# Kernel tuning notes

Hardware: AMD Instinct MI355X
Metric: run time of the kernel (lower is better)

Reference implementation:

```python
import jax, jax.numpy as jnp
import numpy as np

B, S, D, H = 4, 2048, 1024, 16
DEPTH = D // H
NEG = -1000000000.0


def setup_inputs() -> dict:
    key = jax.random.key(0)
    ks = jax.random.split(key, 11)
    scale = 1.0 / np.sqrt(D)
    return {
        "q": jax.random.normal(ks[0], (B, S, D), jnp.float32),
        "k": jax.random.normal(ks[1], (B, S, D), jnp.float32),
        "v": jax.random.normal(ks[2], (B, S, D), jnp.float32),
        "wq_w": jax.random.normal(ks[3], (D, D), jnp.float32) * scale,
        "wq_b": jax.random.normal(ks[4], (D,), jnp.float32) * 0.01,
        "wk_w": jax.random.normal(ks[5], (D, D), jnp.float32) * scale,
        "wk_b": jax.random.normal(ks[6], (D,), jnp.float32) * 0.01,
        "wv_w": jax.random.normal(ks[7], (D, D), jnp.float32) * scale,
        "wv_b": jax.random.normal(ks[8], (D,), jnp.float32) * 0.01,
        "dense_w": jax.random.normal(ks[9], (D, D), jnp.float32) * scale,
        "dense_b": jax.random.normal(ks[10], (D,), jnp.float32) * 0.01,
    }


def _split_heads(x):
    # (B, S, D) -> (B, H, S, depth)
    b, s, _ = x.shape
    return x.reshape(b, s, H, DEPTH).transpose(0, 2, 1, 3)


def reference(q, k, v, wq_w, wq_b, wk_w, wk_b, wv_w, wv_b, dense_w, dense_b):
    b, s, _ = q.shape
    qh = _split_heads(q @ wq_w.T + wq_b)
    kh = _split_heads(k @ wk_w.T + wk_b)
    vh = _split_heads(v @ wv_w.T + wv_b)
    logits = jnp.einsum('bhqd,bhkd->bhqk', qh, kh) / np.sqrt(DEPTH).astype(np.float32)
    # additive causal mask (strict upper triangle = -1e9)
    mask = jnp.where(jnp.triu(jnp.ones((s, s), jnp.float32), k=1) == 1.0, NEG, 0.0)
    logits = logits + mask
    attn = jax.nn.softmax(logits, axis=-1)
    out = jnp.einsum('bhqk,bhkd->bhqd', attn, vh)
    out = out.transpose(0, 2, 1, 3).reshape(b, s, D)
    return out @ dense_w.T + dense_b
```

## Files before the change

### kernel.cpp

```cpp
#include <hip/hip_runtime.h>
#include <hip/hip_bf16.h>


typedef __attribute__((ext_vector_type(8))) short bf16x8;
typedef __attribute__((ext_vector_type(4))) float f32x4;
typedef __attribute__((ext_vector_type(8))) unsigned short u16x8;

#define MFMA16(a, b, c) __builtin_amdgcn_mfma_f32_16x16x32_bf16(a, b, c, 0, 0, 0)

#define GLOAD_LDS16(gp, lp)                                                    \
  __builtin_amdgcn_global_load_lds(                                            \
      (const __attribute__((address_space(1))) void*)(gp),                     \
      (__attribute__((address_space(3))) void*)(lp), 16, 0, 0)

__device__ __forceinline__ unsigned short f2bf(float f) {
  union { float f; unsigned u; } x; x.f = f;
  unsigned u = x.u;
  return (unsigned short)((u + 0x7fffu + ((u >> 16) & 1u)) >> 16);
}

__device__ __forceinline__ unsigned pk2(float a, float b) {
  union { __hip_bfloat162 h; unsigned u; } cv;
  cv.h = __float22bfloat162_rn(float2{a, b});
  return cv.u;
}

__global__ __launch_bounds__(256) void convert_kernel(
    const float* __restrict__ q, const float* __restrict__ k,
    const float* __restrict__ v, const float* __restrict__ wq,
    const float* __restrict__ wk, const float* __restrict__ wv,
    const float* __restrict__ wd, const float* __restrict__ bq,
    const float* __restrict__ bk, const float* __restrict__ bv,
    unsigned short* __restrict__ dst, float* __restrict__ bias_pack) {
  const size_t tid0 = (size_t)blockIdx.x * blockDim.x + threadIdx.x;
  const size_t nthreads = (size_t)gridDim.x * blockDim.x;
  if (tid0 < 3072) {
    bias_pack[tid0] = tid0 < 1024 ? bq[tid0]
                     : (tid0 < 2048 ? bk[tid0 - 1024] : bv[tid0 - 2048]);
  }
  const size_t NQ = 8192ull * 1024;
  const size_t NW = 1024ull * 1024;
  const size_t total_chunks = (3 * NQ + 4 * NW) / 8;
  for (size_t c = tid0; c < total_chunks; c += nthreads) {
    const size_t e = c * 8;
    const float* src;
    if (e < NQ) src = q + e;
    else if (e < 2 * NQ) src = k + (e - NQ);
    else if (e < 3 * NQ) src = v + (e - 2 * NQ);
    else {
      const size_t we = e - 3 * NQ;
      if (we < NW) src = wq + we;
      else if (we < 2 * NW) src = wk + (we - NW);
      else if (we < 3 * NW) src = wv + (we - 2 * NW);
      else src = wd + (we - 3 * NW);
    }
    f32x4 a = *(const f32x4*)(src);
    f32x4 b = *(const f32x4*)(src + 4);
    u16x8 o;
    o[0] = f2bf(a[0]); o[1] = f2bf(a[1]); o[2] = f2bf(a[2]); o[3] = f2bf(a[3]);
    o[4] = f2bf(b[0]); o[5] = f2bf(b[1]); o[6] = f2bf(b[2]); o[7] = f2bf(b[3]);
    *(u16x8*)(dst + e) = o;
  }
}

template <int MODE>
__global__ __launch_bounds__(256) void gemm_kernel(
    const unsigned short* __restrict__ Abase,
    const unsigned short* __restrict__ Wbase,
    const float* __restrict__ biasbase, unsigned short* __restrict__ dstb,
    float* __restrict__ dstf) {
  __shared__ __attribute__((aligned(16))) unsigned short Ablk[128 * 32];
  __shared__ __attribute__((aligned(16))) unsigned short Bblk[128 * 32];
  const int z = blockIdx.z;
  const unsigned short* A = Abase + (size_t)z * (8192ull * 1024);
  const unsigned short* W = Wbase + (size_t)z * (1024ull * 1024);
  const float* bias = biasbase + (size_t)z * 1024;
  const int m0 = blockIdx.y * 128, n0 = blockIdx.x * 128;
  const int tid = threadIdx.x, lane = tid & 63, w = tid >> 6;
  const int wr = (w >> 1) * 64, wc = (w & 1) * 64;
  const int llo = lane & 15, lhi = lane >> 4;
  f32x4 acc[4][4] = {};
  const unsigned short* ag = A + (size_t)(m0 + (tid >> 2)) * 1024 + (tid & 3) * 8;
  const unsigned short* wg = W + (size_t)(n0 + (tid >> 2)) * 1024 + (tid & 3) * 8;
  unsigned short* lA = &Ablk[tid * 8];
  unsigned short* lA2 = &Ablk[2048 + tid * 8];
  unsigned short* lB = &Bblk[tid * 8];
  unsigned short* lB2 = &Bblk[2048 + tid * 8];
  for (int kt = 0; kt < 32; ++kt) {
    const int ko = kt * 32;
    if (kt) __syncthreads();
    GLOAD_LDS16(ag + ko, lA);
    GLOAD_LDS16(ag + ko + 64 * 1024, lA2);
    GLOAD_LDS16(wg + ko, lB);
    GLOAD_LDS16(wg + ko + 64 * 1024, lB2);
    __syncthreads();
    bf16x8 af[4], bfr[4];
#pragma unroll
    for (int i = 0; i < 4; ++i)
      af[i] = *(const bf16x8*)&Ablk[(wr + i * 16 + llo) * 32 + lhi * 8];
#pragma unroll
    for (int i = 0; i < 4; ++i)
      bfr[i] = *(const bf16x8*)&Bblk[(wc + i * 16 + llo) * 32 + lhi * 8];
#pragma unroll
    for (int mi = 0; mi < 4; ++mi)
#pragma unroll
      for (int ni = 0; ni < 4; ++ni)
        acc[mi][ni] = MFMA16(af[mi], bfr[ni], acc[mi][ni]);
  }
  const float osc = (MODE == 0 && z == 0) ? 0.1803368801f : 1.0f;
#pragma unroll
  for (int mi = 0; mi < 4; ++mi) {
#pragma unroll
    for (int ni = 0; ni < 4; ++ni) {
      const int n = n0 + wc + ni * 16 + llo;
      const float bv = (MODE == 2) ? 0.f : bias[n];
#pragma unroll
      for (int r = 0; r < 4; ++r) {
        const int m = m0 + wr + mi * 16 + lhi * 4 + r;
        float val = acc[mi][ni][r] + bv;
        if (MODE == 0) {
          val *= osc;
          const int b = m >> 11, s = m & 2047, h = n >> 6, d = n & 63;
          dstb[(size_t)z * (8192ull * 1024) +
               (((size_t)(b * 16 + h) * 2048 + s) * 64 + d)] = f2bf(val);
        } else if (MODE == 1) {
          dstf[(size_t)m * 1024 + n] = val;
        } else {
          val = acc[mi][ni][r] + bias[m];
          const int h = m >> 6, d = m & 63, b = n >> 11, sidx = n & 2047;
          const int t = sidx & 63;
          const int ps = (sidx & ~63) | ((t & 15) << 2) | (t >> 4);
          dstb[(((size_t)(b * 16 + h) * 64 + d) * 2048 + ps)] = f2bf(val);
        }
      }
    }
  }
}

__global__ __launch_bounds__(256, 4) void attn_kernel(
    const unsigned short* __restrict__ Qp, const unsigned short* __restrict__ Kp,
    const unsigned short* __restrict__ Vtp, unsigned short* __restrict__ attn_out) {
  __shared__ __attribute__((aligned(16))) unsigned short Klds[64 * 64];
  __shared__ __attribute__((aligned(16))) unsigned short Vt[80 * 64];
  __shared__ __attribute__((aligned(16))) unsigned short Plds[4 * 32 * 72];
  const int bh = blockIdx.x;
  const int qt = 15 - blockIdx.y;
  const int tid = threadIdx.x, lane = tid & 63, w = tid >> 6;
  const int llo = lane & 15, lhi = lane >> 4;
  const int q0 = qt * 128;
  const int qbase = q0 + w * 32;

  {
    const unsigned v16 = (tid < 16) ? 0x3F80u : 0u;
    const unsigned vv = v16 | (v16 << 16);
    *(uint2*)&Vt[64 * 64 + tid * 4] = make_uint2(vv, vv);
  }

  bf16x8 qf[2][2];
#pragma unroll
  for (int mi = 0; mi < 2; ++mi) {
    const unsigned short* qptr =
        Qp + ((size_t)bh * 2048 + qbase + mi * 16 + llo) * 64 + lhi * 8;
    qf[mi][0] = *(const bf16x8*)qptr;
    qf[mi][1] = *(const bf16x8*)(qptr + 32);
  }

  f32x4 o[2][5] = {};

  const size_t kbase = (size_t)bh * (64 * 2048);
  const int r0 = tid >> 3, r1 = r0 + 32;
  const int scb = (tid & 7) * 16;
  const int kcol0 = (scb ^ ((r0 & 7) << 4)) >> 1;
  const int kcol1 = (scb ^ ((r1 & 7) << 4)) >> 1;
  const int koff0 = r0 * 64 + kcol0, koff1 = r1 * 64 + kcol1;
  const int voff0 = r0 * 2048 + kcol0, voff1 = r1 * 2048 + kcol1;
  unsigned short* pw = &Plds[w * (32 * 72)];

  const int nkt = 2 * (qt + 1);
  for (int kt = 0; kt < nkt; ++kt) {
    const int kv0 = kt * 64;
    if (kt) __syncthreads();
    GLOAD_LDS16(Kp + kbase + (size_t)kv0 * 64 + koff0, &Klds[tid * 8]);
    GLOAD_LDS16(Kp + kbase + (size_t)kv0 * 64 + koff1, &Klds[2048 + tid * 8]);
    GLOAD_LDS16(Vtp + kbase + kv0 + voff0, &Vt[tid * 8]);
    GLOAD_LDS16(Vtp + kbase + kv0 + voff1, &Vt[2048 + tid * 8]);
    __syncthreads();
    if (kv0 > qbase + 31) continue;

    f32x4 s[2][4] = {};
#pragma unroll
    for (int b4 = 0; b4 < 4; ++b4) {
      const int row = b4 * 16 + llo;
      const int sw = (row & 7) << 3;
      const bf16x8 k0 = *(const bf16x8*)&Klds[row * 64 + ((lhi * 8) ^ sw)];
      const bf16x8 k1 = *(const bf16x8*)&Klds[row * 64 + ((32 + lhi * 8) ^ sw)];
      s[0][b4] = MFMA16(qf[0][0], k0, s[0][b4]);
      s[0][b4] = MFMA16(qf[0][1], k1, s[0][b4]);
      s[1][b4] = MFMA16(qf[1][0], k0, s[1][b4]);
      s[1][b4] = MFMA16(qf[1][1], k1, s[1][b4]);
    }

    const bool needm = (kv0 + 63 > qbase);
#pragma unroll
    for (int mi = 0; mi < 2; ++mi) {
#pragma unroll
      for (int r = 0; r < 4; ++r) {
        float sv0 = s[mi][0][r], sv1 = s[mi][1][r];
        float sv2 = s[mi][2][r], sv3 = s[mi][3][r];
        if (needm) {
          const int qrow = qbase + mi * 16 + lhi * 4 + r;
          if (kv0 + llo > qrow) sv0 = -1e9f;
          if (kv0 + 16 + llo > qrow) sv1 = -1e9f;
          if (kv0 + 32 + llo > qrow) sv2 = -1e9f;
          if (kv0 + 48 + llo > qrow) sv3 = -1e9f;
        }
        const float p0 = exp2f(sv0), p1 = exp2f(sv1);
        const float p2 = exp2f(sv2), p3 = exp2f(sv3);
        const int prow = mi * 16 + lhi * 4 + r;
        *(uint2*)&pw[prow * 72 + llo * 4] = make_uint2(pk2(p0, p1), pk2(p2, p3));
      }
    }

    bf16x8 pa[2][2];
#pragma unroll
    for (int mi = 0; mi < 2; ++mi) {
      pa[mi][0] = *(const bf16x8*)&pw[(mi * 16 + llo) * 72 + lhi * 8];
      pa[mi][1] = *(const bf16x8*)&pw[(mi * 16 + llo) * 72 + 32 + lhi * 8];
    }
#pragma unroll
    for (int dblk = 0; dblk < 5; ++dblk) {
      const int row = dblk * 16 + llo;
      const int sw = (row & 7) << 3;
      const bf16x8 v0 = *(const bf16x8*)&Vt[row * 64 + ((lhi * 8) ^ sw)];
      const bf16x8 v1 = *(const bf16x8*)&Vt[row * 64 + ((32 + lhi * 8) ^ sw)];
      o[0][dblk] = MFMA16(pa[0][0], v0, o[0][dblk]);
      o[0][dblk] = MFMA16(pa[0][1], v1, o[0][dblk]);
      o[1][dblk] = MFMA16(pa[1][0], v0, o[1][dblk]);
      o[1][dblk] = MFMA16(pa[1][1], v1, o[1][dblk]);
    }
  }

  const int b = bh >> 4, h = bh & 15;
#pragma unroll
  for (int mi = 0; mi < 2; ++mi) {
#pragma unroll
    for (int r = 0; r < 4; ++r) {
      const float lsum = __shfl(o[mi][4][r], lane & 48);
      const float inv = 1.0f / lsum;
      const int qrow = qbase + mi * 16 + lhi * 4 + r;
      const size_t base = ((size_t)b * 2048 + qrow) * 1024 + h * 64;
#pragma unroll
      for (int dblk = 0; dblk < 4; ++dblk)
        attn_out[base + dblk * 16 + llo] = f2bf(o[mi][dblk][r] * inv);
    }
  }
}

extern "C" void kernel_launch(void* const* d_in, const int* in_sizes, int n_in,
                              void* d_out, int out_size, void* d_ws,
                              size_t ws_size, hipStream_t stream) {
  const float* q = (const float*)d_in[0];
  const float* k = (const float*)d_in[1];
  const float* v = (const float*)d_in[2];
  const float* wq_w = (const float*)d_in[3];
  const float* wq_b = (const float*)d_in[4];
  const float* wk_w = (const float*)d_in[5];
  const float* wk_b = (const float*)d_in[6];
  const float* wv_w = (const float*)d_in[7];
  const float* wv_b = (const float*)d_in[8];
  const float* dense_w = (const float*)d_in[9];
  const float* dense_b = (const float*)d_in[10];
  float* out = (float*)d_out;

  char* ws = (char*)d_ws;
  const size_t MB = 1024ull * 1024;
  unsigned short* qkv_bf = (unsigned short*)(ws);
  unsigned short* w_bf = (unsigned short*)(ws + 48 * MB);
  float* bias_pack = (float*)(ws + 56 * MB);
  unsigned short* qkvp = (unsigned short*)(ws + 57 * MB);
  unsigned short* attn_o = (unsigned short*)(ws + 105 * MB);
  const size_t PEL = 8192ull * 1024;

  convert_kernel<<<dim3(2048), dim3(256), 0, stream>>>(
      q, k, v, wq_w, wk_w, wv_w, dense_w, wq_b, wk_b, wv_b, qkv_bf, bias_pack);

  gemm_kernel<0><<<dim3(8, 64, 2), dim3(256), 0, stream>>>(
      qkv_bf, w_bf, bias_pack, qkvp, nullptr);

  gemm_kernel<2><<<dim3(64, 8, 1), dim3(256), 0, stream>>>(
      w_bf + 2ull * 1024 * 1024, qkv_bf + 2 * PEL, bias_pack + 2048,
      qkvp + 2 * PEL, nullptr);

  attn_kernel<<<dim3(64, 16), dim3(256), 0, stream>>>(
      qkvp, qkvp + PEL, qkvp + 2 * PEL, attn_o);

  gemm_kernel<1><<<dim3(8, 64, 1), dim3(256), 0, stream>>>(
      attn_o, w_bf + 3ull * 1024 * 1024, dense_b, nullptr, out);
}
```

Measured before the change: 211.9 us.

## Merge V-projection GEMM into QK launch and double attention query tile

The V-projection (transposed-output) GEMM becomes the third z-slice of the Q/K projection launch, with swapped operands and block indices, which removes one kernel launch and lets all three projections share one grid. The attention kernel now handles 256 queries per block (64 per wave) instead of 128. This doubles reuse of each K/V tile loaded into LDS and halves the number of blocks, while the causal grid shrinks from 16 to 8 query tiles. s_setprio hints are added around the MFMA sections; the price is more registers, occupancy bound lowered to 2, and coarser causal load balance.

Result: slower. 243.3 us (+14.9%).

```diff
diff --git a/kernel.cpp b/kernel.cpp
--- a/kernel.cpp
+++ b/kernel.cpp
@@ -71,11 +71,23 @@
     float* __restrict__ dstf) {
   __shared__ __attribute__((aligned(16))) unsigned short Ablk[128 * 32];
   __shared__ __attribute__((aligned(16))) unsigned short Bblk[128 * 32];
+  const size_t NQ = 8192ull * 1024, NW = 1024ull * 1024;
   const int z = blockIdx.z;
-  const unsigned short* A = Abase + (size_t)z * (8192ull * 1024);
-  const unsigned short* W = Wbase + (size_t)z * (1024ull * 1024);
+  const unsigned short* A;
+  const unsigned short* W;
+  int m0, n0;
+  if (MODE == 0 && z == 2) {
+    A = Wbase + 2 * NW;
+    W = Abase + 2 * NQ;
+    m0 = blockIdx.x * 128;
+    n0 = blockIdx.y * 128;
+  } else {
+    A = Abase + (size_t)z * NQ;
+    W = Wbase + (size_t)z * NW;
+    m0 = blockIdx.y * 128;
+    n0 = blockIdx.x * 128;
+  }
   const float* bias = biasbase + (size_t)z * 1024;
-  const int m0 = blockIdx.y * 128, n0 = blockIdx.x * 128;
   const int tid = threadIdx.x, lane = tid & 63, w = tid >> 6;
   const int wr = (w >> 1) * 64, wc = (w & 1) * 64;
   const int llo = lane & 15, lhi = lane >> 4;
@@ -113,42 +125,41 @@
 #pragma unroll
     for (int ni = 0; ni < 4; ++ni) {
       const int n = n0 + wc + ni * 16 + llo;
-      const float bv = (MODE == 2) ? 0.f : bias[n];
+      const float bv = (MODE == 0) ? ((z == 2) ? 0.f : bias[n]) : bias[n];
 #pragma unroll
       for (int r = 0; r < 4; ++r) {
         const int m = m0 + wr + mi * 16 + lhi * 4 + r;
         float val = acc[mi][ni][r] + bv;
-        if (MODE == 0) {
+        if (MODE == 1) {
+          dstf[(size_t)m * 1024 + n] = val;
+        } else if (z < 2) {
           val *= osc;
           const int b = m >> 11, s = m & 2047, h = n >> 6, d = n & 63;
-          dstb[(size_t)z * (8192ull * 1024) +
+          dstb[(size_t)z * NQ +
                (((size_t)(b * 16 + h) * 2048 + s) * 64 + d)] = f2bf(val);
-        } else if (MODE == 1) {
-          dstf[(size_t)m * 1024 + n] = val;
         } else {
           val = acc[mi][ni][r] + bias[m];
           const int h = m >> 6, d = m & 63, b = n >> 11, sidx = n & 2047;
           const int t = sidx & 63;
           const int ps = (sidx & ~63) | ((t & 15) << 2) | (t >> 4);
-          dstb[(((size_t)(b * 16 + h) * 64 + d) * 2048 + ps)] = f2bf(val);
+          dstb[2 * NQ + (((size_t)(b * 16 + h) * 64 + d) * 2048 + ps)] = f2bf(val);
         }
       }
     }
   }
 }
 
-__global__ __launch_bounds__(256, 4) void attn_kernel(
+__global__ __launch_bounds__(256, 2) void attn_kernel(
     const unsigned short* __restrict__ Qp, const unsigned short* __restrict__ Kp,
     const unsigned short* __restrict__ Vtp, unsigned short* __restrict__ attn_out) {
   __shared__ __attribute__((aligned(16))) unsigned short Klds[64 * 64];
   __shared__ __attribute__((aligned(16))) unsigned short Vt[80 * 64];
-  __shared__ __attribute__((aligned(16))) unsigned short Plds[4 * 32 * 72];
+  __shared__ __attribute__((aligned(16))) unsigned short Plds[4 * 64 * 72];
   const int bh = blockIdx.x;
-  const int qt = 15 - blockIdx.y;
+  const int qt = 7 - blockIdx.y;
   const int tid = threadIdx.x, lane = tid & 63, w = tid >> 6;
   const int llo = lane & 15, lhi = lane >> 4;
-  const int q0 = qt * 128;
-  const int qbase = q0 + w * 32;
+  const int qbase = qt * 256 + w * 64;
 
   {
     const unsigned v16 = (tid < 16) ? 0x3F80u : 0u;
@@ -156,16 +167,16 @@
     *(uint2*)&Vt[64 * 64 + tid * 4] = make_uint2(vv, vv);
   }
 
-  bf16x8 qf[2][2];
-#pragma unroll
-  for (int mi = 0; mi < 2; ++mi) {
+  bf16x8 qf[4][2];
+#pragma unroll
+  for (int mi = 0; mi < 4; ++mi) {
     const unsigned short* qptr =
         Qp + ((size_t)bh * 2048 + qbase + mi * 16 + llo) * 64 + lhi * 8;
     qf[mi][0] = *(const bf16x8*)qptr;
     qf[mi][1] = *(const bf16x8*)(qptr + 32);
   }
 
-  f32x4 o[2][5] = {};
+  f32x4 o[4][5] = {};
 
   const size_t kbase = (size_t)bh * (64 * 2048);
   const int r0 = tid >> 3, r1 = r0 + 32;
@@ -174,9 +185,9 @@
   const int kcol1 = (scb ^ ((r1 & 7) << 4)) >> 1;
   const int koff0 = r0 * 64 + kcol0, koff1 = r1 * 64 + kcol1;
   const int voff0 = r0 * 2048 + kcol0, voff1 = r1 * 2048 + kcol1;
-  unsigned short* pw = &Plds[w * (32 * 72)];
-
-  const int nkt = 2 * (qt + 1);
+  unsigned short* pw = &Plds[w * (64 * 72)];
+
+  const int nkt = 4 * (qt + 1);
   for (int kt = 0; kt < nkt; ++kt) {
     const int kv0 = kt * 64;
     if (kt) __syncthreads();
@@ -185,64 +196,73 @@
     GLOAD_LDS16(Vtp + kbase + kv0 + voff0, &Vt[tid * 8]);
     GLOAD_LDS16(Vtp + kbase + kv0 + voff1, &Vt[2048 + tid * 8]);
     __syncthreads();
-    if (kv0 > qbase + 31) continue;
-
-    f32x4 s[2][4] = {};
-#pragma unroll
-    for (int b4 = 0; b4 < 4; ++b4) {
-      const int row = b4 * 16 + llo;
-      const int sw = (row & 7) << 3;
-      const bf16x8 k0 = *(const bf16x8*)&Klds[row * 64 + ((lhi * 8) ^ sw)];
-      const bf16x8 k1 = *(const bf16x8*)&Klds[row * 64 + ((32 + lhi * 8) ^ sw)];
-      s[0][b4] = MFMA16(qf[0][0], k0, s[0][b4]);
-      s[0][b4] = MFMA16(qf[0][1], k1, s[0][b4]);
-      s[1][b4] = MFMA16(qf[1][0], k0, s[1][b4]);
-      s[1][b4] = MFMA16(qf[1][1], k1, s[1][b4]);
-    }
+    if (kv0 > qbase + 63) continue;
 
     const bool needm = (kv0 + 63 > qbase);
 #pragma unroll
-    for (int mi = 0; mi < 2; ++mi) {
-#pragma unroll
-      for (int r = 0; r < 4; ++r) {
-        float sv0 = s[mi][0][r], sv1 = s[mi][1][r];
-        float sv2 = s[mi][2][r], sv3 = s[mi][3][r];
-        if (needm) {
-          const int qrow = qbase + mi * 16 + lhi * 4 + r;
-          if (kv0 + llo > qrow) sv0 = -1e9f;
-          if (kv0 + 16 + llo > qrow) sv1 = -1e9f;
-          if (kv0 + 32 + llo > qrow) sv2 = -1e9f;
-          if (kv0 + 48 + llo > qrow) sv3 = -1e9f;
+    for (int half = 0; half < 2; ++half) {
+      f32x4 s[2][4] = {};
+      __builtin_amdgcn_s_setprio(1);
+#pragma unroll
+      for (int b4 = 0; b4 < 4; ++b4) {
+        const int row = b4 * 16 + llo;
+        const int sw = (row & 7) << 3;
+        const bf16x8 k0 = *(const bf16x8*)&Klds[row * 64 + ((lhi * 8) ^ sw)];
+        const bf16x8 k1 = *(const bf16x8*)&Klds[row * 64 + ((32 + lhi * 8) ^ sw)];
+#pragma unroll
+        for (int j = 0; j < 2; ++j) {
+          s[j][b4] = MFMA16(qf[half * 2 + j][0], k0, s[j][b4]);
+          s[j][b4] = MFMA16(qf[half * 2 + j][1], k1, s[j][b4]);
         }
-        const float p0 = exp2f(sv0), p1 = exp2f(sv1);
-        const float p2 = exp2f(sv2), p3 = exp2f(sv3);
-        const int prow = mi * 16 + lhi * 4 + r;
-        *(uint2*)&pw[prow * 72 + llo * 4] = make_uint2(pk2(p0, p1), pk2(p2, p3));
       }
-    }
-
-    bf16x8 pa[2][2];
-#pragma unroll
-    for (int mi = 0; mi < 2; ++mi) {
+      __builtin_amdgcn_s_setprio(0);
+#pragma unroll
+      for (int j = 0; j < 2; ++j) {
+#pragma unroll
+        for (int r = 0; r < 4; ++r) {
+          float sv0 = s[j][0][r], sv1 = s[j][1][r];
+          float sv2 = s[j][2][r], sv3 = s[j][3][r];
+          if (needm) {
+            const int qrow = qbase + (half * 2 + j) * 16 + lhi * 4 + r;
+            if (kv0 + llo > qrow) sv0 = -1e9f;
+            if (kv0 + 16 + llo > qrow) sv1 = -1e9f;
+            if (kv0 + 32 + llo > qrow) sv2 = -1e9f;
+            if (kv0 + 48 + llo > qrow) sv3 = -1e9f;
+          }
+          const float p0 = exp2f(sv0), p1 = exp2f(sv1);
+          const float p2 = exp2f(sv2), p3 = exp2f(sv3);
+          const int prow = (half * 2 + j) * 16 + lhi * 4 + r;
+          *(uint2*)&pw[prow * 72 + llo * 4] =
+              make_uint2(pk2(p0, p1), pk2(p2, p3));
+        }
+      }
+    }
+
+    bf16x8 pa[4][2];
+#pragma unroll
+    for (int mi = 0; mi < 4; ++mi) {
       pa[mi][0] = *(const bf16x8*)&pw[(mi * 16 + llo) * 72 + lhi * 8];
       pa[mi][1] = *(const bf16x8*)&pw[(mi * 16 + llo) * 72 + 32 + lhi * 8];
     }
+    __builtin_amdgcn_s_setprio(1);
 #pragma unroll
     for (int dblk = 0; dblk < 5; ++dblk) {
       const int row = dblk * 16 + llo;
       const int sw = (row & 7) << 3;
       const bf16x8 v0 = *(const bf16x8*)&Vt[row * 64 + ((lhi * 8) ^ sw)];
       const bf16x8 v1 = *(const bf16x8*)&Vt[row * 64 + ((32 + lhi * 8) ^ sw)];
-      o[0][dblk] = MFMA16(pa[0][0], v0, o[0][dblk]);
-      o[0][dblk] = MFMA16(pa[0][1], v1, o[0][dblk]);
-      o[1][dblk] = MFMA16(pa[1][0], v0, o[1][dblk]);
-      o[1][dblk] = MFMA16(pa[1][1], v1, o[1][dblk]);
-    }
+#pragma unroll
+      for (int mi = 0; mi < 4; ++mi) {
+        o[mi][dblk] = MFMA16(pa[mi][0], v0, o[mi][dblk]);
+        o[mi][dblk] = MFMA16(pa[mi][1], v1, o[mi][dblk]);
+      }
+    }
+    __builtin_amdgcn_s_setprio(0);
   }
 
   const int b = bh >> 4, h = bh & 15;
 #pragma unroll
-  for (int mi = 0; mi < 2; ++mi) {
+  for (int mi = 0; mi < 4; ++mi) {
 #pragma unroll
     for (int r = 0; r < 4; ++r) {
       const float lsum = __shfl(o[mi][4][r], lane & 48);
@@ -284,14 +304,10 @@
   convert_kernel<<<dim3(2048), dim3(256), 0, stream>>>(
       q, k, v, wq_w, wk_w, wv_w, dense_w, wq_b, wk_b, wv_b, qkv_bf, bias_pack);
 
-  gemm_kernel<0><<<dim3(8, 64, 2), dim3(256), 0, stream>>>(
+  gemm_kernel<0><<<dim3(8, 64, 3), dim3(256), 0, stream>>>(
       qkv_bf, w_bf, bias_pack, qkvp, nullptr);
 
-  gemm_kernel<2><<<dim3(64, 8, 1), dim3(256), 0, stream>>>(
-      w_bf + 2ull * 1024 * 1024, qkv_bf + 2 * PEL, bias_pack + 2048,
-      qkvp + 2 * PEL, nullptr);
-
-  attn_kernel<<<dim3(64, 16), dim3(256), 0, stream>>>(
+  attn_kernel<<<dim3(64, 8), dim3(256), 0, stream>>>(
       qkvp, qkvp + PEL, qkvp + 2 * PEL, attn_o);
 
   gemm_kernel<1><<<dim3(8, 64, 1), dim3(256), 0, stream>>>(
```
